# Optimization experiments

Measured on AMD Instinct MI355X. Metric: run time of the kernel, lower is better.

Reference implementation:

```python
import jax, jax.numpy as jnp
import numpy as np

N, M = 100000, 12          # atoms, neighbors per atom
ORIG, F, NBR, H = 92, 64, 41, 128
NC = 3                     # n_conv
C = 3125                   # crystals
EPS = 1e-5                 # BatchNorm eps (torch default)


def setup_inputs() -> dict:
    key = jax.random.key(0)
    ks = jax.random.split(key, 8)
    w = lambda k, s: jax.random.normal(k, s, jnp.float32) * 0.05
    return {
        "atom_fea": jax.random.normal(ks[0], (N, ORIG), jnp.float32),
        "nbr_fea": jax.random.normal(ks[1], (N, M, NBR), jnp.float32),
        "nbr_fea_idx": jax.random.randint(ks[2], (N, M), 0, N),
        "seg_ids": jnp.sort(jax.random.randint(ks[3], (N,), 0, C)),
        "n_crystals": C,
        "mask": jnp.ones((ORIG,), jnp.float32),
        "embW": w(ks[4], (ORIG, F)), "embb": jnp.zeros((F,), jnp.float32),
        "fcW": w(ks[5], (NC, 2 * F + NBR, 2 * F)), "fcb": jnp.zeros((NC, 2 * F), jnp.float32),
        "bn1g": jnp.ones((NC, 2 * F), jnp.float32), "bn1b": jnp.zeros((NC, 2 * F), jnp.float32),
        "bn2g": jnp.ones((NC, F), jnp.float32), "bn2b": jnp.zeros((NC, F), jnp.float32),
        "c2fW": w(ks[6], (F, H)), "c2fb": jnp.zeros((H,), jnp.float32),
        "outW": w(ks[7], (H, 1)), "outb": jnp.zeros((1,), jnp.float32),
    }


def _bn(x, g, b):
    # BatchNorm1d in training mode: biased batch stats over dim 0
    mu = x.mean(0)
    var = x.var(0)
    return (x - mu) * jax.lax.rsqrt(var + EPS) * g + b


def reference(atom_fea, nbr_fea, nbr_fea_idx, seg_ids, n_crystals, mask,
              embW, embb, fcW, fcb, bn1g, bn1b, bn2g, bn2b,
              c2fW, c2fb, outW, outb):
    x = (atom_fea * mask) @ embW + embb              # [N, F]
    for l in range(NC):                              # fixed small layer loop
        nbr = x[nbr_fea_idx]                         # [N, M, F] gather
        self_f = jnp.broadcast_to(x[:, None, :], (N, M, F))
        tot = jnp.concatenate([self_f, nbr, nbr_fea], axis=-1)   # [N, M, 2F+NBR]
        g = tot @ fcW[l] + fcb[l]                    # [N, M, 2F]
        g = _bn(g.reshape(N * M, 2 * F), bn1g[l], bn1b[l]).reshape(N, M, 2 * F)
        filt, core = g[..., :F], g[..., F:]
        summed = jnp.sum(jax.nn.sigmoid(filt) * jax.nn.softplus(core), axis=1)  # [N, F]
        x = jax.nn.softplus(x + _bn(summed, bn2g[l], bn2b[l]))
    # per-crystal mean pooling (segment ids replace list of index maps)
    sums = jax.ops.segment_sum(x, seg_ids, num_segments=n_crystals)
    cnt = jax.ops.segment_sum(jnp.ones((N,), x.dtype), seg_ids, num_segments=n_crystals)
    crys = sums / jnp.maximum(cnt, 1.0)[:, None]     # [C, F]
    crys = jax.nn.softplus(jax.nn.softplus(crys) @ c2fW + c2fb)  # [C, H]
    return crys @ outW + outb                        # [C, 1]
```

## Files before the change

kernel.cpp:

```cpp
#include <hip/hip_runtime.h>
#include <hip/hip_bf16.h>


#define NN    100000
#define MM    12
#define ORIG  92
#define FF    64
#define NBR   41
#define HH    128
#define NCONV 3
#define CC    3125
#define K2    169
#define GG    128
#define EPSV  1e-5f

#define TILE_ATOMS 8
#define TILE_ROWS  96
#define NTILES     (NN / TILE_ATOMS)
#define SLOTS      24
#define WPK_L      (48 * 64 * 8)
#define CONV_GRID  750
#define ETILES     1563
#define PCHUNK_ROWS 128
#define PCHUNK_F32  (PCHUNK_ROWS * NBR)
#define PCHUNK_U4   (PCHUNK_F32 / 4)
#define NPCHUNK     ((NN * MM) / PCHUNK_ROWS)
#define LOG2E_F    1.44269504088896341f
#define LN2_F      0.69314718055994531f

typedef __attribute__((ext_vector_type(8))) short bf16x8;
typedef __attribute__((ext_vector_type(4))) float f32x4;

__device__ __forceinline__ float softplusf(float v) {
    return fmaxf(v, 0.f) + log1pf(expf(-fabsf(v)));
}
__device__ __forceinline__ float sigmoidf_(float v) {
    return 1.f / (1.f + expf(-v));
}
__device__ __forceinline__ ushort f2bf(float f) {
    __hip_bfloat16 h = __float2bfloat16(f);
    return *(ushort*)&h;
}
__device__ __forceinline__ float bf2f(ushort h) {
    uint u = ((uint)h) << 16;
    return __uint_as_float(u);
}
__device__ __forceinline__ void gload_lds16(const void* gsrc, void* ldst) {
    __builtin_amdgcn_global_load_lds(
        (const __attribute__((address_space(1))) unsigned int*)gsrc,
        (__attribute__((address_space(3))) unsigned int*)ldst, 16, 0, 0);
}

__global__ void packWemb_kernel(const float* __restrict__ embW, const float* __restrict__ mask,
                                ushort* __restrict__ wemb) {
    int b = blockIdx.x;
    int cf = b / 3;
    int kk = b - cf * 3;
    int lane = threadIdx.x;
    int c = cf * 16 + (lane & 15);
#pragma unroll
    for (int i = 0; i < 8; i++) {
        int k = kk * 32 + (lane >> 4) * 8 + i;
        float v = (k < ORIG) ? mask[k] * embW[k * FF + c] : 0.f;
        wemb[((size_t)b * 64 + lane) * 8 + i] = f2bf(v);
    }
}

__launch_bounds__(256)
__global__ void embed_mfma(const float* __restrict__ af, const ushort* __restrict__ wemb,
                           const float* __restrict__ embb,
                           float* __restrict__ x, ushort* __restrict__ xb) {
    __shared__ __align__(16) ushort Ae[64 * 128];
    const int t = threadIdx.x;
    const int lane = t & 63;
    const int w = t >> 6;
    const int l15 = lane & 15;
    const int lg = lane >> 4;
    const int a0 = blockIdx.x * 64;

    bf16x8 bfrag[4][3];
#pragma unroll
    for (int cf = 0; cf < 4; cf++)
#pragma unroll
        for (int kk = 0; kk < 3; kk++)
            bfrag[cf][kk] = *(const bf16x8*)&wemb[(((size_t)(cf * 3 + kk)) * 64 + lane) * 8];

#pragma unroll
    for (int uu = 0; uu < 3; uu++) {
        int u = uu * 256 + t;
        int row = u / 12;
        int slot = u - row * 12;
        int a = a0 + row;
        if (a >= NN) a = NN - 1;
        const float* src = af + (size_t)a * ORIG + slot * 8;
        float v[8];
        float4 p0 = *(const float4*)src;
        v[0] = p0.x; v[1] = p0.y; v[2] = p0.z; v[3] = p0.w;
        if (slot < 11) {
            float4 p1 = *(const float4*)(src + 4);
            v[4] = p1.x; v[5] = p1.y; v[6] = p1.z; v[7] = p1.w;
        } else {
            v[4] = v[5] = v[6] = v[7] = 0.f;
        }
        uint4 val;
        val.x = (uint)f2bf(v[0]) | ((uint)f2bf(v[1]) << 16);
        val.y = (uint)f2bf(v[2]) | ((uint)f2bf(v[3]) << 16);
        val.z = (uint)f2bf(v[4]) | ((uint)f2bf(v[5]) << 16);
        val.w = (uint)f2bf(v[6]) | ((uint)f2bf(v[7]) << 16);
        *(uint4*)&Ae[row * 128 + ((slot ^ (row & 7)) * 8)] = val;
    }
    __syncthreads();

    f32x4 acc[4];
#pragma unroll
    for (int cf = 0; cf < 4; cf++) acc[cf] = (f32x4){0.f, 0.f, 0.f, 0.f};

#pragma unroll
    for (int kk = 0; kk < 3; kk++) {
        int row = w * 16 + l15;
        int slot = kk * 4 + lg;
        bf16x8 a = *(const bf16x8*)&Ae[row * 128 + ((slot ^ (row & 7)) * 8)];
#pragma unroll
        for (int cf = 0; cf < 4; cf++)
            acc[cf] = __builtin_amdgcn_mfma_f32_16x16x32_bf16(a, bfrag[cf][kk], acc[cf], 0, 0, 0);
    }

#pragma unroll
    for (int cf = 0; cf < 4; cf++) {
        int c = cf * 16 + l15;
        float bb = embb[c];
#pragma unroll
        for (int q = 0; q < 4; q++) {
            int a = a0 + w * 16 + lg * 4 + q;
            if (a < NN) {
                float v = acc[cf][q] + bb;
                x[(size_t)a * FF + c] = v;
                xb[(size_t)a * FF + c] = f2bf(v);
            }
        }
    }
}

__global__ void packW_kernel(const float* __restrict__ fcW, ushort* __restrict__ wpk) {
    int b = blockIdx.x;
    int l = b / 48;
    int r = b - l * 48;
    int cf = r / 6;
    int kk = r - cf * 6;
    int lane = threadIdx.x;
    int c = cf * 16 + (lane & 15);
#pragma unroll
    for (int i = 0; i < 8; i++) {
        int k = kk * 32 + (lane >> 4) * 8 + i;
        float v = (k < K2) ? fcW[(l * K2 + k) * GG + c] : 0.f;
        wpk[((size_t)b * 64 + lane) * 8 + i] = f2bf(v);
    }
}

__launch_bounds__(256)
__global__ void prepack_nbr(const float* __restrict__ nbr_fea, ushort* __restrict__ nbrb) {
    __shared__ float buf[PCHUNK_F32];
    const int t = threadIdx.x;
    for (int chunk = blockIdx.x; chunk < NPCHUNK; chunk += gridDim.x) {
        const uint4* src = (const uint4*)(nbr_fea + (size_t)chunk * PCHUNK_F32);
        __syncthreads();
#pragma unroll
        for (int i = 0; i < 6; i++) {
            int u = i * 256 + t;
            if (u < PCHUNK_U4) *(uint4*)&buf[u * 4] = src[u];
        }
        __syncthreads();
#pragma unroll
        for (int i = 0; i < 4; i++) {
            int u = i * 256 + t;
            int row = u >> 3;
            int kb = (u & 7) * 8;
            ushort h[8];
#pragma unroll
            for (int j = 0; j < 8; j++)
                h[j] = (kb + j < NBR) ? f2bf(buf[row * NBR + kb + j]) : (ushort)0;
            uint4 val;
            val.x = (uint)h[0] | ((uint)h[1] << 16);
            val.y = (uint)h[2] | ((uint)h[3] << 16);
            val.z = (uint)h[4] | ((uint)h[5] << 16);
            val.w = (uint)h[6] | ((uint)h[7] << 16);
            *(uint4*)&nbrb[((size_t)chunk * PCHUNK_ROWS + row) * 64 + kb] = val;
        }
    }
}

template <int MODE>
__launch_bounds__(256, 3)
__global__ void conv_fused(const ushort* __restrict__ xb, const ushort* __restrict__ nbrb,
                           const int* __restrict__ nidx, const ushort* __restrict__ wpk_l,
                           const float* __restrict__ fcb_l,
                           float* __restrict__ stats,
                           const float* __restrict__ sc1, const float* __restrict__ sh1,
                           float* __restrict__ summed, float* __restrict__ stats2) {
    __shared__ __align__(16) ushort As[3][TILE_ROWS * 64];
    __shared__ int nbstage[2][TILE_ROWS];
    __shared__ float red[256];

    const int t = threadIdx.x;
    const int lane = t & 63;
    const int w = t >> 6;
    const int l15 = lane & 15;
    const int lg = lane >> 4;

    bf16x8 bfrag[2][6];
#pragma unroll
    for (int c2 = 0; c2 < 2; c2++)
#pragma unroll
        for (int kk = 0; kk < 6; kk++)
            bfrag[c2][kk] = *(const bf16x8*)&wpk_l[((((w + 4 * c2) * 6 + kk) * 64 + lane) * 8)];

    const int chF = w * 16 + l15;
    float scF = 0.f, shF = 0.f, scC = 0.f, shC = 0.f;
    if (MODE == 1) {
        scF = sc1[chF]; shF = sh1[chF];
        scC = sc1[chF + 64]; shC = sh1[chF + 64];
    }

    float sAF = 0.f, sBF = 0.f, sAC = 0.f, sBC = 0.f;
    float s2a = 0.f, s2b = 0.f;

    int pt = t; if (pt >= TILE_ROWS) pt -= TILE_ROWS; if (pt >= TILE_ROWS) pt -= TILE_ROWS;
    const int pidx = (pt & 7) * MM + (pt >> 3);

    int rowi[3], sli[3];
#pragma unroll
    for (int i = 0; i < 3; i++) {
        int u = w * 192 + i * 64 + lane;
        rowi[i] = u >> 3;
        sli[i] = (u & 7) ^ (rowi[i] & 7);
    }
    const ushort* p0p[3];
    const ushort* p2p[3];
#pragma unroll
    for (int i = 0; i < 3; i++) {
        p0p[i] = xb + ((size_t)blockIdx.x * TILE_ATOMS + (rowi[i] & 7)) * 64 + sli[i] * 8;
        p2p[i] = nbrb + ((size_t)blockIdx.x * TILE_ROWS + (rowi[i] & 7) * MM + (rowi[i] >> 3)) * 64
                 + sli[i] * 8;
    }
    const size_t st0 = (size_t)CONV_GRID * TILE_ATOMS * 64;
    const size_t st2 = (size_t)CONV_GRID * TILE_ROWS * 64;

    auto issue0 = [&]() {
#pragma unroll
        for (int i = 0; i < 3; i++) {
            gload_lds16(p0p[i], &As[0][(w * 192 + i * 64) * 8]);
            p0p[i] += st0;
        }
    };
    auto issue1 = [&](int nb) {
#pragma unroll
        for (int i = 0; i < 3; i++)
            gload_lds16(xb + (size_t)nbstage[nb][rowi[i]] * 64 + sli[i] * 8,
                        &As[1][(w * 192 + i * 64) * 8]);
    };
    auto issue2 = [&]() {
#pragma unroll
        for (int i = 0; i < 3; i++) {
            gload_lds16(p2p[i], &As[2][(w * 192 + i * 64) * 8]);
            p2p[i] += st2;
        }
    };

    int tile = blockIdx.x;
    int idx_cur;
    {
        int nx0 = nidx[tile * TILE_ROWS + pidx];
        int nx1 = nidx[(tile + CONV_GRID) * TILE_ROWS + pidx];
        if (t < TILE_ROWS) { nbstage[0][t] = nx0; nbstage[1][t] = nx1; }
        __syncthreads();
        idx_cur = nidx[(tile + 2 * CONV_GRID) * TILE_ROWS + pidx];
        issue0(); issue1(0); issue2();
        asm volatile("" ::: "memory");
    }

    for (int it = 0; tile < NTILES; tile += CONV_GRID, ++it) {
        const bool have1 = (tile + CONV_GRID)     < NTILES;
        const bool have2 = (tile + 2 * CONV_GRID) < NTILES;
        const bool have3 = (tile + 3 * CONV_GRID) < NTILES;

        int idx_next = 0;
        if (have3) idx_next = nidx[(tile + 3 * CONV_GRID) * TILE_ROWS + pidx];

        f32x4 acc[6][2];
#pragma unroll
        for (int rf = 0; rf < 6; rf++)
#pragma unroll
            for (int c2 = 0; c2 < 2; c2++) acc[rf][c2] = (f32x4){0.f, 0.f, 0.f, 0.f};

        if (it == 0)       { asm volatile("s_waitcnt vmcnt(4)"  ::: "memory"); }
        else if (have3) {
            if (MODE == 1) { asm volatile("s_waitcnt vmcnt(8)"  ::: "memory"); }
            else           { asm volatile("s_waitcnt vmcnt(4)"  ::: "memory"); }
        } else {
            if (MODE == 1) { asm volatile("s_waitcnt vmcnt(7)"  ::: "memory"); }
            else           { asm volatile("s_waitcnt vmcnt(3)"  ::: "memory"); }
        }
        __builtin_amdgcn_s_barrier();
        __builtin_amdgcn_sched_barrier(0);
#pragma unroll
        for (int sb = 0; sb < 2; sb++) {
#pragma unroll
            for (int kx = 0; kx < 2; kx++) {
                int kk = sb * 2 + kx;
#pragma unroll
                for (int rf = 0; rf < 6; rf++) {
                    int row = rf * 16 + l15;
                    int s8r = kx * 4 + lg;
                    bf16x8 a = *(const bf16x8*)&As[sb][row * 64 + ((s8r ^ (row & 7)) * 8)];
                    acc[rf][0] = __builtin_amdgcn_mfma_f32_16x16x32_bf16(a, bfrag[0][kk], acc[rf][0], 0, 0, 0);
                    acc[rf][1] = __builtin_amdgcn_mfma_f32_16x16x32_bf16(a, bfrag[1][kk], acc[rf][1], 0, 0, 0);
                }
            }
        }
        asm volatile("" ::: "memory");
        __builtin_amdgcn_s_barrier();
        if (have1) { issue0(); issue1((it + 1) & 1); }
        asm volatile("" ::: "memory");

        if (it == 0)            { asm volatile("s_waitcnt vmcnt(7)" ::: "memory"); }
        else if (have1 && have3){ asm volatile("s_waitcnt vmcnt(7)" ::: "memory"); }
        else if (have1)         { asm volatile("s_waitcnt vmcnt(6)" ::: "memory"); }
        else                    { asm volatile("s_waitcnt vmcnt(0)" ::: "memory"); }
        __builtin_amdgcn_s_barrier();
        __builtin_amdgcn_sched_barrier(0);
#pragma unroll
        for (int kx = 0; kx < 2; kx++) {
            int kk = 4 + kx;
#pragma unroll
            for (int rf = 0; rf < 6; rf++) {
                int row = rf * 16 + l15;
                int s8r = kx * 4 + lg;
                bf16x8 a = *(const bf16x8*)&As[2][row * 64 + ((s8r ^ (row & 7)) * 8)];
                acc[rf][0] = __builtin_amdgcn_mfma_f32_16x16x32_bf16(a, bfrag[0][kk], acc[rf][0], 0, 0, 0);
                acc[rf][1] = __builtin_amdgcn_mfma_f32_16x16x32_bf16(a, bfrag[1][kk], acc[rf][1], 0, 0, 0);
            }
        }

        if (MODE == 0) {
#pragma unroll
            for (int rf = 0; rf < 6; rf++)
#pragma unroll
                for (int q = 0; q < 4; q++) {
                    float a0 = acc[rf][0][q];
                    float a1 = acc[rf][1][q];
                    sAF += a0; sBF = fmaf(a0, a0, sBF);
                    sAC += a1; sBC = fmaf(a1, a1, sBC);
                }
        } else {
            float psum[4] = {0.f, 0.f, 0.f, 0.f};
#pragma unroll
            for (int rf = 0; rf < 6; rf++)
#pragma unroll
                for (int q = 0; q < 4; q++) {
                    float gF = fmaf(acc[rf][0][q], scF, shF);
                    float gC = fmaf(acc[rf][1][q], scC, shC);
                    float sig = __builtin_amdgcn_rcpf(1.f + __builtin_amdgcn_exp2f(-gF));
                    float sp  = fmaxf(gC, 0.f)
                              + __builtin_amdgcn_logf(1.f + __builtin_amdgcn_exp2f(-fabsf(gC)));
                    psum[q] = fmaf(sig, sp, psum[q]);
                }
#pragma unroll
            for (int q = 0; q < 4; q++) {
                psum[q] *= LN2_F;
                psum[q] += __shfl_xor(psum[q], 32, 64);
            }
            if (lg < 2) {
                int atom0 = tile * TILE_ATOMS;
#pragma unroll
                for (int q = 0; q < 4; q++) {
                    int a_loc = (lg & 1) * 4 + q;
                    float sm = psum[q];
                    summed[(size_t)(atom0 + a_loc) * FF + chF] = sm;
                    s2a += sm; s2b += sm * sm;
                }
            }
        }

        if (have2 && t < TILE_ROWS) nbstage[it & 1][t] = idx_cur;
        idx_cur = idx_next;
        asm volatile("s_waitcnt lgkmcnt(0)" ::: "memory");
        __builtin_amdgcn_s_barrier();
        if (have1) issue2();
        asm volatile("" ::: "memory");
    }

    if (MODE == 0) {
        __syncthreads(); red[t] = sAF; __syncthreads();
        if (t < 64) {
            float s = 0.f;
#pragma unroll
            for (int g2 = 0; g2 < 4; g2++) s += red[(t >> 4) * 64 + g2 * 16 + (t & 15)];
            atomicAdd(&stats[t], s);
        }
        __syncthreads(); red[t] = sBF; __syncthreads();
        if (t < 64) {
            float s = 0.f;
#pragma unroll
            for (int g2 = 0; g2 < 4; g2++) s += red[(t >> 4) * 64 + g2 * 16 + (t & 15)];
            atomicAdd(&stats[128 + t], s);
        }
        __syncthreads(); red[t] = sAC; __syncthreads();
        if (t < 64) {
            float s = 0.f;
#pragma unroll
            for (int g2 = 0; g2 < 4; g2++) s += red[(t >> 4) * 64 + g2 * 16 + (t & 15)];
            atomicAdd(&stats[64 + t], s);
        }
        __syncthreads(); red[t] = sBC; __syncthreads();
        if (t < 64) {
            float s = 0.f;
#pragma unroll
            for (int g2 = 0; g2 < 4; g2++) s += red[(t >> 4) * 64 + g2 * 16 + (t & 15)];
            atomicAdd(&stats[192 + t], s);
        }
    } else {
        __syncthreads(); red[t] = s2a; __syncthreads();
        if (t < 64) {
            float s = 0.f;
#pragma unroll
            for (int g2 = 0; g2 < 4; g2++) s += red[(t >> 4) * 64 + g2 * 16 + (t & 15)];
            atomicAdd(&stats2[t], s);
        }
        __syncthreads(); red[t] = s2b; __syncthreads();
        if (t < 64) {
            float s = 0.f;
#pragma unroll
            for (int g2 = 0; g2 < 4; g2++) s += red[(t >> 4) * 64 + g2 * 16 + (t & 15)];
            atomicAdd(&stats2[64 + t], s);
        }
    }
}

template <int PASS>
__launch_bounds__(256, 2)
__global__ void conv_mfma(const ushort* __restrict__ xb, const float* __restrict__ nbr_fea,
                          const int* __restrict__ nidx, const ushort* __restrict__ wpk_l,
                          const float* __restrict__ fcb_l,
                          float* __restrict__ stats,
                          const float* __restrict__ sc1, const float* __restrict__ sh1,
                          float* __restrict__ summed, float* __restrict__ stats2) {
    __shared__ __align__(16) ushort As[TILE_ROWS * 192];
    __shared__ int nb[TILE_ROWS];
    __shared__ float gacc[TILE_ATOMS * FF];
    __shared__ float red[256];

    const int t = threadIdx.x;
    const int lane = t & 63;
    const int w = t >> 6;
    const int l15 = lane & 15;
    const int lg = lane >> 4;

    bf16x8 bfrag[2][6];
#pragma unroll
    for (int c2 = 0; c2 < 2; c2++)
#pragma unroll
        for (int kk = 0; kk < 6; kk++)
            bfrag[c2][kk] = *(const bf16x8*)&wpk_l[((((w + 4 * c2) * 6 + kk) * 64 + lane) * 8)];

    const int chF = w * 16 + l15;
    const int chC = chF + 64;
    const float bF = fcb_l[chF], bC = fcb_l[chC];
    float scF = 0.f, shF = 0.f, scC = 0.f, shC = 0.f;
    if (PASS == 1) { scF = sc1[chF]; shF = sh1[chF]; scC = sc1[chC]; shC = sh1[chC]; }

    float sAF = 0.f, sBF = 0.f, sAC = 0.f, sBC = 0.f;
    float s2a = 0.f, s2b = 0.f;

    for (int tile = blockIdx.x; tile < NTILES; tile += gridDim.x) {
        const int ebase = tile * TILE_ROWS;
        __syncthreads();
        if (t < TILE_ROWS) nb[t] = nidx[ebase + t];
        if (PASS == 1) { gacc[t] = 0.f; gacc[256 + t] = 0.f; }
        __syncthreads();

#pragma unroll
        for (int e = t; e < TILE_ROWS * SLOTS; e += 256) {
            int row = e / SLOTS;
            int slot = e - row * SLOTS;
            uint4 val;
            if (slot < 16) {
                int a = (slot < 8) ? (tile * TILE_ATOMS + row / 12) : nb[row];
                val = *(const uint4*)&xb[a * 64 + (slot & 7) * 8];
            } else {
                int kb = (slot - 16) * 8;
                const float* src = nbr_fea + (size_t)(ebase + row) * NBR + kb;
                ushort h[8];
#pragma unroll
                for (int i = 0; i < 8; i++)
                    h[i] = (kb + i < NBR) ? f2bf(src[i]) : (ushort)0;
                val.x = (uint)h[0] | ((uint)h[1] << 16);
                val.y = (uint)h[2] | ((uint)h[3] << 16);
                val.z = (uint)h[4] | ((uint)h[5] << 16);
                val.w = (uint)h[6] | ((uint)h[7] << 16);
            }
            *(uint4*)&As[row * 192 + ((slot ^ (row & 7)) * 8)] = val;
        }
        __syncthreads();

        f32x4 acc[6][2];
#pragma unroll
        for (int rf = 0; rf < 6; rf++)
#pragma unroll
            for (int c2 = 0; c2 < 2; c2++) acc[rf][c2] = (f32x4){0.f, 0.f, 0.f, 0.f};

#pragma unroll
        for (int kk = 0; kk < 6; kk++) {
#pragma unroll
            for (int rf = 0; rf < 6; rf++) {
                int row = rf * 16 + l15;
                int slot = kk * 4 + lg;
                bf16x8 a = *(const bf16x8*)&As[row * 192 + ((slot ^ (row & 7)) * 8)];
                acc[rf][0] = __builtin_amdgcn_mfma_f32_16x16x32_bf16(a, bfrag[0][kk], acc[rf][0], 0, 0, 0);
                acc[rf][1] = __builtin_amdgcn_mfma_f32_16x16x32_bf16(a, bfrag[1][kk], acc[rf][1], 0, 0, 0);
            }
        }

        if (PASS == 0) {
#pragma unroll
            for (int rf = 0; rf < 6; rf++)
#pragma unroll
                for (int q = 0; q < 4; q++) {
                    float a0 = acc[rf][0][q];
                    float a1 = acc[rf][1][q];
                    sAF += a0; sBF = fmaf(a0, a0, sBF);
                    sAC += a1; sBC = fmaf(a1, a1, sBC);
                }
        } else {
#pragma unroll
            for (int rf = 0; rf < 6; rf++) {
                int r0 = rf * 16 + lg * 4;
                float p = 0.f;
#pragma unroll
                for (int q = 0; q < 4; q++) {
                    float gF = (acc[rf][0][q] + bF) * scF + shF;
                    float gC = (acc[rf][1][q] + bC) * scC + shC;
                    p += sigmoidf_(gF) * softplusf(gC);
                }
                atomicAdd(&gacc[(r0 / 12) * FF + chF], p);
            }
            __syncthreads();
#pragma unroll
            for (int rep = 0; rep < 2; rep++) {
                int idx = rep * 256 + t;
                int a = idx >> 6, c = idx & 63;
                float sm = gacc[idx];
                summed[(tile * TILE_ATOMS + a) * FF + c] = sm;
                s2a += sm; s2b += sm * sm;
            }
        }
    }

    if (PASS == 0) {
        __syncthreads(); red[t] = sAF; __syncthreads();
        if (t < 64) {
            float s = 0.f;
#pragma unroll
            for (int g2 = 0; g2 < 4; g2++) s += red[(t >> 4) * 64 + g2 * 16 + (t & 15)];
            atomicAdd(&stats[t], s);
        }
        __syncthreads(); red[t] = sBF; __syncthreads();
        if (t < 64) {
            float s = 0.f;
#pragma unroll
            for (int g2 = 0; g2 < 4; g2++) s += red[(t >> 4) * 64 + g2 * 16 + (t & 15)];
            atomicAdd(&stats[128 + t], s);
        }
        __syncthreads(); red[t] = sAC; __syncthreads();
        if (t < 64) {
            float s = 0.f;
#pragma unroll
            for (int g2 = 0; g2 < 4; g2++) s += red[(t >> 4) * 64 + g2 * 16 + (t & 15)];
            atomicAdd(&stats[64 + t], s);
        }
        __syncthreads(); red[t] = sBC; __syncthreads();
        if (t < 64) {
            float s = 0.f;
#pragma unroll
            for (int g2 = 0; g2 < 4; g2++) s += red[(t >> 4) * 64 + g2 * 16 + (t & 15)];
            atomicAdd(&stats[192 + t], s);
        }
    } else {
        __syncthreads(); red[t] = s2a; __syncthreads();
        if (t < 64) {
            float s = red[t] + red[64 + t] + red[128 + t] + red[192 + t];
            atomicAdd(&stats2[t], s);
        }
        __syncthreads(); red[t] = s2b; __syncthreads();
        if (t < 64) {
            float s = red[t] + red[64 + t] + red[128 + t] + red[192 + t];
            atomicAdd(&stats2[64 + t], s);
        }
    }
}

__global__ void fin1_kernel(const float* __restrict__ stats, const float* __restrict__ fcb_l,
                            const float* __restrict__ g, const float* __restrict__ b,
                            float* __restrict__ sc, float* __restrict__ sh, int fold) {
    int c = threadIdx.x;
    const float inv = 1.f / (float)(NN * MM);
    float bia = fcb_l[c];
    float Sa = stats[c], Sb = stats[128 + c];
    float mu = Sa * inv + bia;
    float ex2 = (Sb + 2.f * bia * Sa) * inv + bia * bia;
    float var = ex2 - mu * mu;
    float s = rsqrtf(var + EPSV) * g[c];
    float scv = s;
    float shv = b[c] - mu * s;
    if (fold) { scv *= LOG2E_F; shv *= LOG2E_F; }
    sc[c] = scv;
    sh[c] = shv;
}

__global__ void fin2_kernel(const float* __restrict__ stats2, const float* __restrict__ g,
                            const float* __restrict__ b, float* __restrict__ sc, float* __restrict__ sh) {
    int c = threadIdx.x;
    const float inv = 1.f / (float)NN;
    float mu = stats2[c] * inv;
    float var = stats2[64 + c] * inv - mu * mu;
    float s = rsqrtf(var + EPSV) * g[c];
    sc[c] = s;
    sh[c] = b[c] - mu * s;
}

__global__ void update_x_kernel(float* __restrict__ x, ushort* __restrict__ xb,
                                const float* __restrict__ summed,
                                const float* __restrict__ sc2, const float* __restrict__ sh2) {
    for (int idx = blockIdx.x * blockDim.x + threadIdx.x; idx < NN * FF;
         idx += gridDim.x * blockDim.x) {
        int c = idx & 63;
        float v = softplusf(x[idx] + summed[idx] * sc2[c] + sh2[c]);
        x[idx] = v;
        xb[idx] = f2bf(v);
    }
}

__global__ void update_x_pool_kernel(const float* __restrict__ x,
                                     const float* __restrict__ summed,
                                     const float* __restrict__ sc2, const float* __restrict__ sh2,
                                     const int* __restrict__ seg,
                                     float* __restrict__ csum, float* __restrict__ ccnt) {
    for (int idx = blockIdx.x * blockDim.x + threadIdx.x; idx < NN * FF;
         idx += gridDim.x * blockDim.x) {
        int i = idx >> 6;
        int c = idx & 63;
        float v = softplusf(x[idx] + summed[idx] * sc2[c] + sh2[c]);
        atomicAdd(&csum[seg[i] * FF + c], v);
        if (c == 0) atomicAdd(&ccnt[seg[i]], 1.f);
    }
}

__global__ void head_kernel(const float* __restrict__ csum, const float* __restrict__ ccnt,
                            const float* __restrict__ c2fW, const float* __restrict__ c2fb,
                            const float* __restrict__ outW, const float* __restrict__ outb,
                            float* __restrict__ out) {
    __shared__ float pl[FF];
    __shared__ float red[HH];
    int c = blockIdx.x;
    int t = threadIdx.x;
    if (t < FF) {
        float cnt = fmaxf(ccnt[c], 1.f);
        pl[t] = softplusf(csum[c * FF + t] / cnt);
    }
    __syncthreads();
    float acc = c2fb[t];
    for (int f = 0; f < FF; f++) acc += pl[f] * c2fW[f * HH + t];
    red[t] = softplusf(acc) * outW[t];
    __syncthreads();
    for (int s = 64; s > 0; s >>= 1) {
        if (t < s) red[t] += red[t + s];
        __syncthreads();
    }
    if (t == 0) out[c] = red[0] + outb[0];
}

extern "C" void kernel_launch(void* const* d_in, const int* in_sizes, int n_in,
                              void* d_out, int out_size, void* d_ws, size_t ws_size,
                              hipStream_t stream) {
    const float* atom_fea = (const float*)d_in[0];
    const float* nbr_fea  = (const float*)d_in[1];
    const int*   nbr_idx  = (const int*)d_in[2];
    const int*   seg      = (const int*)d_in[3];
    const float* mask = (const float*)d_in[5];
    const float* embW = (const float*)d_in[6];
    const float* embb = (const float*)d_in[7];
    const float* fcW  = (const float*)d_in[8];
    const float* fcb  = (const float*)d_in[9];
    const float* bn1g = (const float*)d_in[10];
    const float* bn1b = (const float*)d_in[11];
    const float* bn2g = (const float*)d_in[12];
    const float* bn2b = (const float*)d_in[13];
    const float* c2fW = (const float*)d_in[14];
    const float* c2fb = (const float*)d_in[15];
    const float* outW = (const float*)d_in[16];
    const float* outb = (const float*)d_in[17];
    float* out = (float*)d_out;

    float* ws     = (float*)d_ws;
    float* x      = ws;
    float* summed = x + NN * FF;
    float* csum   = summed + NN * FF;
    float* ccnt   = csum + CC * FF;
    float* stats  = ccnt + 3128;
    float* stats2 = stats + 256;
    float* sc1    = stats2 + 128;
    float* sh1    = sc1 + 128;
    float* sc2    = sh1 + 128;
    float* sh2    = sc2 + 64;
    ushort* xb    = (ushort*)(sh2 + 64);
    ushort* wpk   = xb + NN * FF;
    ushort* wemb  = wpk + 3 * WPK_L;
    ushort* nbrb  = wemb + 8192;

    const size_t need_full =
        (size_t)((char*)(nbrb + (size_t)NN * MM * 64) - (char*)d_ws);
    const bool full = (ws_size >= need_full);

    packW_kernel<<<144, 64, 0, stream>>>(fcW, wpk);
    packWemb_kernel<<<12, 64, 0, stream>>>(embW, mask, wemb);
    embed_mfma<<<ETILES, 256, 0, stream>>>(atom_fea, wemb, embb, x, xb);
    if (full) prepack_nbr<<<2048, 256, 0, stream>>>(nbr_fea, nbrb);
    hipMemsetAsync(csum, 0, (CC * FF + CC) * sizeof(float), stream);

    for (int l = 0; l < NCONV; l++) {
        const ushort* wpk_l = wpk + l * WPK_L;
        hipMemsetAsync(stats, 0, (256 + 128) * sizeof(float), stream);
        if (full) {
            conv_fused<0><<<CONV_GRID, 256, 0, stream>>>(xb, nbrb, nbr_idx, wpk_l,
                                                         fcb + l * GG, stats,
                                                         nullptr, nullptr, nullptr, nullptr);
            fin1_kernel<<<1, 128, 0, stream>>>(stats, fcb + l * GG,
                                               bn1g + l * GG, bn1b + l * GG, sc1, sh1, 1);
            conv_fused<1><<<CONV_GRID, 256, 0, stream>>>(xb, nbrb, nbr_idx, wpk_l,
                                                         fcb + l * GG, nullptr,
                                                         sc1, sh1, summed, stats2);
        } else {
            conv_mfma<0><<<2048, 256, 0, stream>>>(xb, nbr_fea, nbr_idx, wpk_l, fcb + l * GG,
                                                   stats, nullptr, nullptr, nullptr, nullptr);
            fin1_kernel<<<1, 128, 0, stream>>>(stats, fcb + l * GG,
                                               bn1g + l * GG, bn1b + l * GG, sc1, sh1, 0);
            conv_mfma<1><<<2048, 256, 0, stream>>>(xb, nbr_fea, nbr_idx, wpk_l, fcb + l * GG,
                                                   nullptr, sc1, sh1, summed, stats2);
        }
        fin2_kernel<<<1, 64, 0, stream>>>(stats2, bn2g + l * FF, bn2b + l * FF, sc2, sh2);
        if (l < NCONV - 1) {
            update_x_kernel<<<2048, 256, 0, stream>>>(x, xb, summed, sc2, sh2);
        } else {
            update_x_pool_kernel<<<2048, 256, 0, stream>>>(x, summed, sc2, sh2,
                                                           seg, csum, ccnt);
        }
    }

    head_kernel<<<CC, 128, 0, stream>>>(csum, ccnt, c2fW, c2fb, outW, outb, out);
}
```

Before: 715.8 us.

## Double-buffer the neighbor-feature LDS tile and merge the conv MFMA phases

Adds a fourth LDS buffer so the nbr_fea slice (As[2]) is double-buffered and prefetched two tiles ahead. This removes the mid-iteration barrier and wait between the self/neighbor MFMAs and the nbr_fea MFMAs, so all three K-chunks run in one loop. All next-tile loads are now issued together at the end of the iteration. The cost is more shared memory per block, which may reduce occupancy at 3 blocks per CU. The rewritten vmcnt accounting must exactly match the new issue order.

```diff
diff --git a/kernel.cpp b/kernel.cpp
--- a/kernel.cpp
+++ b/kernel.cpp
@@ -197,7 +197,7 @@
                            float* __restrict__ stats,
                            const float* __restrict__ sc1, const float* __restrict__ sh1,
                            float* __restrict__ summed, float* __restrict__ stats2) {
-    __shared__ __align__(16) ushort As[3][TILE_ROWS * 64];
+    __shared__ __align__(16) ushort As[4][TILE_ROWS * 64];
     __shared__ int nbstage[2][TILE_ROWS];
     __shared__ float red[256];
 
@@ -258,10 +258,10 @@
             gload_lds16(xb + (size_t)nbstage[nb][rowi[i]] * 64 + sli[i] * 8,
                         &As[1][(w * 192 + i * 64) * 8]);
     };
-    auto issue2 = [&]() {
+    auto issue2 = [&](int pb) {
 #pragma unroll
         for (int i = 0; i < 3; i++) {
-            gload_lds16(p2p[i], &As[2][(w * 192 + i * 64) * 8]);
+            gload_lds16(p2p[i], &As[2 + pb][(w * 192 + i * 64) * 8]);
             p2p[i] += st2;
         }
     };
@@ -274,7 +274,8 @@
         if (t < TILE_ROWS) { nbstage[0][t] = nx0; nbstage[1][t] = nx1; }
         __syncthreads();
         idx_cur = nidx[(tile + 2 * CONV_GRID) * TILE_ROWS + pidx];
-        issue0(); issue1(0); issue2();
+        issue0(); issue1(0); issue2(0);
+        if (tile + CONV_GRID < NTILES) issue2(1);
         asm volatile("" ::: "memory");
     }
 
@@ -282,28 +283,26 @@
         const bool have1 = (tile + CONV_GRID)     < NTILES;
         const bool have2 = (tile + 2 * CONV_GRID) < NTILES;
         const bool have3 = (tile + 3 * CONV_GRID) < NTILES;
+        const int pb = it & 1;
 
         int idx_next = 0;
         if (have3) idx_next = nidx[(tile + 3 * CONV_GRID) * TILE_ROWS + pidx];
 
-        f32x4 acc[6][2];
-#pragma unroll
-        for (int rf = 0; rf < 6; rf++)
-#pragma unroll
-            for (int c2 = 0; c2 < 2; c2++) acc[rf][c2] = (f32x4){0.f, 0.f, 0.f, 0.f};
-
-        if (it == 0)       { asm volatile("s_waitcnt vmcnt(4)"  ::: "memory"); }
-        else if (have3) {
-            if (MODE == 1) { asm volatile("s_waitcnt vmcnt(8)"  ::: "memory"); }
-            else           { asm volatile("s_waitcnt vmcnt(4)"  ::: "memory"); }
-        } else {
-            if (MODE == 1) { asm volatile("s_waitcnt vmcnt(7)"  ::: "memory"); }
-            else           { asm volatile("s_waitcnt vmcnt(3)"  ::: "memory"); }
-        }
+        if (!have1)     { asm volatile("s_waitcnt vmcnt(0)" ::: "memory"); }
+        else if (have3) { asm volatile("s_waitcnt vmcnt(4)" ::: "memory"); }
+        else            { asm volatile("s_waitcnt vmcnt(3)" ::: "memory"); }
         __builtin_amdgcn_s_barrier();
         __builtin_amdgcn_sched_barrier(0);
-#pragma unroll
-        for (int sb = 0; sb < 2; sb++) {
+
+        f32x4 acc[6][2];
+#pragma unroll
+        for (int rf = 0; rf < 6; rf++)
+#pragma unroll
+            for (int c2 = 0; c2 < 2; c2++) acc[rf][c2] = (f32x4){0.f, 0.f, 0.f, 0.f};
+
+#pragma unroll
+        for (int sb = 0; sb < 3; sb++) {
+            const ushort* Ab = (sb < 2) ? As[sb] : As[2 + pb];
 #pragma unroll
             for (int kx = 0; kx < 2; kx++) {
                 int kk = sb * 2 + kx;
@@ -311,33 +310,10 @@
                 for (int rf = 0; rf < 6; rf++) {
                     int row = rf * 16 + l15;
                     int s8r = kx * 4 + lg;
-                    bf16x8 a = *(const bf16x8*)&As[sb][row * 64 + ((s8r ^ (row & 7)) * 8)];
+                    bf16x8 a = *(const bf16x8*)&Ab[row * 64 + ((s8r ^ (row & 7)) * 8)];
                     acc[rf][0] = __builtin_amdgcn_mfma_f32_16x16x32_bf16(a, bfrag[0][kk], acc[rf][0], 0, 0, 0);
                     acc[rf][1] = __builtin_amdgcn_mfma_f32_16x16x32_bf16(a, bfrag[1][kk], acc[rf][1], 0, 0, 0);
                 }
-            }
-        }
-        asm volatile("" ::: "memory");
-        __builtin_amdgcn_s_barrier();
-        if (have1) { issue0(); issue1((it + 1) & 1); }
-        asm volatile("" ::: "memory");
-
-        if (it == 0)            { asm volatile("s_waitcnt vmcnt(7)" ::: "memory"); }
-        else if (have1 && have3){ asm volatile("s_waitcnt vmcnt(7)" ::: "memory"); }
-        else if (have1)         { asm volatile("s_waitcnt vmcnt(6)" ::: "memory"); }
-        else                    { asm volatile("s_waitcnt vmcnt(0)" ::: "memory"); }
-        __builtin_amdgcn_s_barrier();
-        __builtin_amdgcn_sched_barrier(0);
-#pragma unroll
-        for (int kx = 0; kx < 2; kx++) {
-            int kk = 4 + kx;
-#pragma unroll
-            for (int rf = 0; rf < 6; rf++) {
-                int row = rf * 16 + l15;
-                int s8r = kx * 4 + lg;
-                bf16x8 a = *(const bf16x8*)&As[2][row * 64 + ((s8r ^ (row & 7)) * 8)];
-                acc[rf][0] = __builtin_amdgcn_mfma_f32_16x16x32_bf16(a, bfrag[0][kk], acc[rf][0], 0, 0, 0);
-                acc[rf][1] = __builtin_amdgcn_mfma_f32_16x16x32_bf16(a, bfrag[1][kk], acc[rf][1], 0, 0, 0);
             }
         }
 
@@ -385,7 +361,12 @@
         idx_cur = idx_next;
         asm volatile("s_waitcnt lgkmcnt(0)" ::: "memory");
         __builtin_amdgcn_s_barrier();
-        if (have1) issue2();
+
+        if (have1) {
+            issue0();
+            issue1((it + 1) & 1);
+            if (have2) issue2(pb);
+        }
         asm volatile("" ::: "memory");
     }
 
```

Measured after the change: 731.3 us. 2.2% more time.
